# Kernel tuning notes

Measured on AMD Instinct MI355X. Metric: run time of the kernel, lower is better.

Reference implementation:

```python
import jax, jax.numpy as jnp
import numpy as np

# ---- static config (mirrors init_kwargs) ----
B, T, H, W = 1, 3, 64, 64
NHEADS, CH = 4, 64
DIM = NHEADS * CH            # 256 = embed_dim*nheads*dim_mult
PS, WS = 7, 9                # patch size, search window
WSH = WS // 2
K_S, K_A = 16, 8             # search top-k, aggregation top-k
S0 = 2                       # stride0: query grid stride
SCALE = CH ** -0.5
NH, NW = (H - 1) // S0 + 1, (W - 1) // S0 + 1
Q = T * NH * NW              # ntotal queries


def reflect_idx(i, n):
    # dnls reflect_bounds: i<0 -> -i, i>=n -> 2(n-1)-i
    i = jnp.where(i < 0, -i, i)
    return jnp.where(i >= n, 2 * (n - 1) - i, i)


def sepconv(x, dw, pw, b):
    # ConvQKV branch: depthwise 3x3 + pointwise 1x1 (+bias). x: [N,C,H,W]
    y = jax.lax.conv_general_dilated(x, dw, (1, 1), 'SAME',
            dimension_numbers=('NCHW', 'OIHW', 'NCHW'),
            feature_group_count=x.shape[1])
    y = jax.lax.conv_general_dilated(y, pw, (1, 1), 'SAME',
            dimension_numbers=('NCHW', 'OIHW', 'NCHW'))
    return y + b[None, :, None, None]


def setup_inputs() -> dict:
    key = jax.random.key(0)
    ks = jax.random.split(key, 12)
    p = lambda k, s, sc=0.02: jax.random.normal(k, s, jnp.float32) * sc
    z = lambda s: jnp.zeros(s, jnp.float32)
    return {
        'vid':  jax.random.normal(ks[0], (B, T, DIM, H, W), jnp.float32),
        'q_dw': p(ks[1], (DIM, 1, 3, 3), 0.1), 'q_pw': p(ks[2], (DIM, DIM, 1, 1)), 'q_b': z((DIM,)),
        'k_dw': p(ks[3], (DIM, 1, 3, 3), 0.1), 'k_pw': p(ks[4], (DIM, DIM, 1, 1)), 'k_b': z((DIM,)),
        'v_dw': p(ks[5], (DIM, 1, 3, 3), 0.1), 'v_pw': p(ks[6], (DIM, DIM, 1, 1)), 'v_b': z((DIM,)),
        'proj_w': p(ks[7], (DIM, DIM)), 'proj_b': z((DIM,)),
    }


def reference(vid, q_dw, q_pw, q_b, k_dw, k_pw, k_b, v_dw, v_pw, v_b, proj_w, proj_b):
    x = vid.reshape(B * T, DIM, H, W)
    q = (sepconv(x, q_dw, q_pw, q_b) * SCALE).reshape(B, T, NHEADS, CH, H, W)
    k = sepconv(x, k_dw, k_pw, k_b).reshape(B, T, NHEADS, CH, H, W)
    v = sepconv(x, v_dw, v_pw, v_b).reshape(B, T, NHEADS, CH, H, W)

    # ---- non-local patch search (prod_with_heads), spatial window ws x ws, wt=0 ----
    yi, xi = jnp.arange(H), jnp.arange(W)
    ye = reflect_idx(jnp.arange(H + PS - 1), H)   # reflect-extended patch footprint
    xe = reflect_idx(jnp.arange(W + PS - 1), W)

    def offset_dists(dyo, dxo):
        # pixelwise q.k for k shifted by (dyo,dxo) with reflect bounds
        ks_ = k[..., reflect_idx(yi + dyo, H), :][..., reflect_idx(xi + dxo, W)]
        d = jnp.sum(q * ks_, axis=3)              # [B,T,HD,H,W]
        # separable ps x ps patch box-sum (patch anchored top-left)
        de = d[..., ye, :][..., xe]               # [B,T,HD,H+PS-1,W+PS-1]
        dsy = sum(de[..., p:p + H, :] for p in range(PS))
        return sum(dsy[..., p:p + W] for p in range(PS))   # [B,T,HD,H,W]

    offs = jnp.arange(WS) - WSH
    dyg, dxg = jnp.meshgrid(offs, offs, indexing='ij')
    dists_all = jax.vmap(offset_dists)(dyg.ravel(), dxg.ravel())  # [L,B,T,HD,H,W]

    gy, gx = jnp.arange(0, H, S0), jnp.arange(0, W, S0)
    dg = dists_all[..., gy, :][..., gx]           # [L,B,T,HD,NH,NW]
    dists = dg.transpose(1, 3, 2, 4, 5, 0).reshape(B, NHEADS, Q, WS * WS)
    vals, inds = jax.lax.top_k(dists, K_S)        # descending
    attn = jax.nn.softmax(vals, axis=-1)[..., :K_A]  # softmax over k_s, keep top k_a
    inds = inds[..., :K_A]

    # ---- weighted patch sum (wpsum) ----
    tq = jnp.repeat(jnp.arange(T), NH * NW)       # query coords [Q]
    yq = jnp.tile(jnp.repeat(gy, NW), T)
    xq = jnp.tile(jnp.tile(gx, NH), T)
    py = jnp.arange(PS)

    vflat = v.transpose(0, 2, 3, 1, 4, 5).reshape(B, NHEADS, CH, T * H * W)
    dy_k = inds // WS - WSH
    dx_k = inds % WS - WSH

    def gather_bh(vf, li):
        # vf: [CH, T*H*W], li: [Q,PS,PS] -> [CH,Q,PS,PS]
        return vf[:, li]

    acc = jnp.zeros((B, NHEADS, CH, Q, PS, PS), vid.dtype)
    for n in range(K_A):  # small fixed loop over neighbors
        yy = reflect_idx((yq[None, None, :] + dy_k[..., n])[..., None] + py, H)  # [B,HD,Q,PS]
        xx = reflect_idx((xq[None, None, :] + dx_k[..., n])[..., None] + py, W)
        lin = tq[None, None, :, None, None] * (H * W) + yy[..., :, None] * W + xx[..., None, :]
        vp = jax.vmap(jax.vmap(gather_bh))(vflat, lin)        # [B,HD,CH,Q,PS,PS]
        acc = acc + attn[..., n][:, :, None, :, None, None] * vp

    # ---- proj over concatenated heads per (query, patch pixel) ----
    pf = acc.transpose(0, 3, 4, 5, 1, 2).reshape(-1, DIM)     # [(B Q PS PS), DIM]
    pf = pf @ proj_w.T + proj_b

    # ---- iFoldz: overlap-add + per-pixel normalization ----
    patches = pf.reshape(B, Q, PS, PS, DIM).transpose(0, 4, 1, 2, 3)  # [B,DIM,Q,PS,PS]
    yyf = reflect_idx(yq[:, None] + py, H)
    xxf = reflect_idx(xq[:, None] + py, W)
    linf = (tq[:, None, None] * (H * W) + yyf[:, :, None] * W + xxf[:, None, :]).ravel()
    vacc = jnp.zeros((B, DIM, T * H * W), vid.dtype).at[:, :, linf].add(patches.reshape(B, DIM, -1))
    zv = jnp.zeros((T * H * W,), vid.dtype).at[linf].add(1.0)
    out = (vacc / zv).reshape(B, DIM, T, H, W).transpose(0, 2, 1, 3, 4)  # [B,T,DIM,H,W]
    return out
```

## Files before the change

kernel.cpp:

```cpp
#include <hip/hip_runtime.h>
#include <hip/hip_bf16.h>
#include <cmath>

#define TT 3
#define HH 64
#define WW 64
#define NPIX 4096
#define NHEADS 4
#define CHD 64
#define DIMD 256
#define PS 7
#define WS 9
#define WSH 4
#define KS 16
#define KA 8
#define NG 32
#define QTOT 3072
#define NOFF 81
#define SCALE 0.125f

#define OFF_DW   ((size_t)0)
#define OFF_Q    ((size_t)9437184)
#define OFF_K    ((size_t)12582912)
#define OFF_V    ((size_t)15728640)
#define OFF_D    ((size_t)18874368)
#define OFF_DG   ((size_t)22855680)
#define OFF_ATTN ((size_t)23851008)
#define OFF_INDS ((size_t)23949312)
#define OFF_VACC ((size_t)24047616)

__device__ __forceinline__ int reflect_i(int i, int n) {
  i = i < 0 ? -i : i;
  return i >= n ? 2 * (n - 1) - i : i;
}

__global__ void k_dw(const float* __restrict__ vid,
                     const float* __restrict__ qdw, const float* __restrict__ kdw,
                     const float* __restrict__ vdw, float* __restrict__ dw) {
  int plane = blockIdx.x;
  int ch = plane & 255;
  const float* src = vid + (size_t)plane * NPIX;
  float wq[9], wk[9], wv[9];
#pragma unroll
  for (int i = 0; i < 9; i++) { wq[i] = qdw[ch*9+i]; wk[i] = kdw[ch*9+i]; wv[i] = vdw[ch*9+i]; }
  int x = threadIdx.x, ty = threadIdx.y;
  for (int yb = 0; yb < 16; ++yb) {
    int y = yb * 4 + ty;
    float aq = 0, ak = 0, av = 0;
#pragma unroll
    for (int a = 0; a < 3; a++) {
      int yy = y + a - 1;
      if (yy < 0 || yy >= HH) continue;
#pragma unroll
      for (int b = 0; b < 3; b++) {
        int xx = x + b - 1;
        if (xx < 0 || xx >= WW) continue;
        float xv = src[yy * WW + xx];
        aq += xv * wq[a*3+b]; ak += xv * wk[a*3+b]; av += xv * wv[a*3+b];
      }
    }
    size_t o = (size_t)plane * NPIX + y * WW + x;
    dw[o] = aq;
    dw[(size_t)3145728 + o] = ak;
    dw[(size_t)6291456 + o] = av;
  }
}

__global__ void k_pw(const float* __restrict__ dw,
                     const float* __restrict__ qpw, const float* __restrict__ qb,
                     const float* __restrict__ kpw, const float* __restrict__ kb,
                     const float* __restrict__ vpw, const float* __restrict__ vb,
                     float* __restrict__ qo, float* __restrict__ ko, float* __restrict__ vo) {
  int type = blockIdx.z / 3, t = blockIdx.z % 3;
  const float* W   = type == 0 ? qpw : (type == 1 ? kpw : vpw);
  const float* bia = type == 0 ? qb  : (type == 1 ? kb  : vb);
  const float* A = dw + (size_t)type * 3145728 + (size_t)t * 1048576;
  int p0 = blockIdx.x * 64, o0 = blockIdx.y * 64;

  __shared__ float sW[2][16][68];
  __shared__ float sA[2][16][68];

  int tid = threadIdx.x;
  int ty = tid >> 4, tx = tid & 15;
  int wrow = tid >> 2, wcol = tid & 3;
  int arow = tid >> 4, acol = tid & 15;

  const float* Wp = &W[(size_t)(o0 + wrow) * 256 + wcol * 4];
  const float* Ap = &A[(size_t)arow * NPIX + p0 + acol * 4];

  {
    float4 w4 = *(const float4*)Wp;
    float4 a4 = *(const float4*)Ap;
    sW[0][wcol * 4 + 0][wrow] = w4.x;
    sW[0][wcol * 4 + 1][wrow] = w4.y;
    sW[0][wcol * 4 + 2][wrow] = w4.z;
    sW[0][wcol * 4 + 3][wrow] = w4.w;
    *(float4*)&sA[0][arow][acol * 4] = a4;
  }
  float4 wH = *(const float4*)(Wp + 16);
  float4 aH = *(const float4*)(Ap + (size_t)16 * NPIX);
  __syncthreads();

  float acc[4][4] = {};

#pragma unroll 1
  for (int k0 = 0; k0 < 256; k0 += 16) {
    const int cur = (k0 >> 4) & 1;
    float4 wN, aN;
    if (k0 + 32 < 256) {
      wN = *(const float4*)(Wp + k0 + 32);
      aN = *(const float4*)(Ap + (size_t)(k0 + 32) * NPIX);
    }
#pragma unroll
    for (int kk = 0; kk < 16; kk++) {
      float4 av = *(const float4*)&sW[cur][kk][ty * 4];
      float4 bv = *(const float4*)&sA[cur][kk][tx * 4];
      acc[0][0] += av.x * bv.x; acc[0][1] += av.x * bv.y; acc[0][2] += av.x * bv.z; acc[0][3] += av.x * bv.w;
      acc[1][0] += av.y * bv.x; acc[1][1] += av.y * bv.y; acc[1][2] += av.y * bv.z; acc[1][3] += av.y * bv.w;
      acc[2][0] += av.z * bv.x; acc[2][1] += av.z * bv.y; acc[2][2] += av.z * bv.z; acc[2][3] += av.z * bv.w;
      acc[3][0] += av.w * bv.x; acc[3][1] += av.w * bv.y; acc[3][2] += av.w * bv.z; acc[3][3] += av.w * bv.w;
    }
    if (k0 + 16 < 256) {
      const int nxt = cur ^ 1;
      sW[nxt][wcol * 4 + 0][wrow] = wH.x;
      sW[nxt][wcol * 4 + 1][wrow] = wH.y;
      sW[nxt][wcol * 4 + 2][wrow] = wH.z;
      sW[nxt][wcol * 4 + 3][wrow] = wH.w;
      *(float4*)&sA[nxt][arow][acol * 4] = aH;
      __syncthreads();
      wH = wN; aH = aN;
    }
  }

  int obase = o0 + ty * 4, pbase = p0 + tx * 4;
  if (type == 2) {
#pragma unroll
    for (int j = 0; j < 4; j++) {
      float4 ov = make_float4(acc[0][j] + bia[obase + 0],
                              acc[1][j] + bia[obase + 1],
                              acc[2][j] + bia[obase + 2],
                              acc[3][j] + bia[obase + 3]);
      *(float4*)&vo[((size_t)t * NPIX + pbase + j) * 256 + obase] = ov;
    }
  } else {
    float* dst = (type == 0) ? qo : ko;
    float sc = (type == 0) ? SCALE : 1.0f;
#pragma unroll
    for (int i = 0; i < 4; i++) {
      float bb = bia[obase + i];
      float4 ov = make_float4((acc[i][0] + bb) * sc, (acc[i][1] + bb) * sc,
                              (acc[i][2] + bb) * sc, (acc[i][3] + bb) * sc);
      *(float4*)&dst[((size_t)t * 256 + obase + i) * NPIX + pbase] = ov;
    }
  }
}

__global__ void k_dist(const float* __restrict__ q, const float* __restrict__ k,
                       float* __restrict__ D) {
  int b = blockIdx.x;
  int y = b & 63, th = b >> 6;
  int t = th >> 2, h = th & 3;
  __shared__ float4 sK4[16][64];
  int tid = threadIdx.x;
  int x = tid & 63, w = tid >> 6;
  const float* qp = q + ((size_t)t * 256 + h * 64) * NPIX + y * WW;
  const float* kp = k + ((size_t)t * 256 + h * 64) * NPIX;

  float4 qv[16];
#pragma unroll
  for (int cc = 0; cc < 16; cc++) {
    qv[cc].x = qp[(size_t)(4 * cc + 0) * NPIX + x];
    qv[cc].y = qp[(size_t)(4 * cc + 1) * NPIX + x];
    qv[cc].z = qp[(size_t)(4 * cc + 2) * NPIX + x];
    qv[cc].w = qp[(size_t)(4 * cc + 3) * NPIX + x];
  }

  for (int dyi = 0; dyi < 9; ++dyi) {
    int yk = reflect_i(y + dyi - 4, HH);
    __syncthreads();
    {
      int cc = tid >> 6;
      const float* kr = kp + (size_t)yk * WW;
#pragma unroll
      for (int r = 0; r < 4; r++) {
        int c4 = (cc + 4 * r) * 4;
        float4 kv;
        kv.x = kr[(size_t)(c4 + 0) * NPIX + x];
        kv.y = kr[(size_t)(c4 + 1) * NPIX + x];
        kv.z = kr[(size_t)(c4 + 2) * NPIX + x];
        kv.w = kr[(size_t)(c4 + 3) * NPIX + x];
        sK4[cc + 4 * r][x] = kv;
      }
    }
    __syncthreads();
    for (int dxi = w; dxi < 9; dxi += 4) {
      int xk = reflect_i(x + dxi - 4, WW);
      float s0 = 0.f, s1 = 0.f, s2 = 0.f, s3 = 0.f;
#pragma unroll
      for (int cc = 0; cc < 16; cc++) {
        float4 kv = sK4[cc][xk];
        s0 += qv[cc].x * kv.x;
        s1 += qv[cc].y * kv.y;
        s2 += qv[cc].z * kv.z;
        s3 += qv[cc].w * kv.w;
      }
      D[((size_t)(dyi * 9 + dxi) * 12 + th) * NPIX + y * WW + x] = (s0 + s1) + (s2 + s3);
    }
  }
}

__global__ void k_box(const float* __restrict__ D, float* __restrict__ DG) {
  int th = blockIdx.x, n = blockIdx.y;
  int t = th >> 2, h = th & 3;
  __shared__ float sD[4096];
  __shared__ float sR[64][33];
  int tid = threadIdx.x;
  const float* Dp = D + ((size_t)n * 12 + th) * NPIX;
  for (int i = tid; i < 4096; i += 256) sD[i] = Dp[i];
  __syncthreads();
  for (int e = tid; e < 2048; e += 256) {
    int y = e >> 5, gx = e & 31;
    int xq = gx * 2;
    const float* row = sD + y * WW;
    float s = 0.f;
#pragma unroll
    for (int px = 0; px < 7; px++) {
      int rx = xq + px; rx = rx >= WW ? 126 - rx : rx;
      s += row[rx];
    }
    sR[y][gx] = s;
  }
  __syncthreads();
  for (int qi = tid; qi < 1024; qi += 256) {
    int gy = qi >> 5, gx = qi & 31;
    int yq = gy * 2;
    float s = 0.f;
#pragma unroll
    for (int py = 0; py < 7; py++) {
      int ry = yq + py; ry = ry >= HH ? 126 - ry : ry;
      s += sR[ry][gx];
    }
    DG[((size_t)h * QTOT + t * 1024 + qi) * NOFF + n] = s;
  }
}

__global__ void k_topk(const float* __restrict__ DG, float* __restrict__ attn,
                       int* __restrict__ inds) {
  int lane = threadIdx.x & 63;
  int r = blockIdx.x * 4 + (threadIdx.x >> 6);
  const float* row = DG + (size_t)r * NOFF;

  float v0 = row[lane];
  float v1 = (lane < NOFF - 64) ? row[64 + lane] : 0.f;

  auto mono = [](float f) -> unsigned {
    unsigned b = __float_as_uint(f);
    return (b & 0x80000000u) ? ~b : (b | 0x80000000u);
  };
  unsigned long long k0 = ((unsigned long long)mono(v0) << 7) | (unsigned)(127 - lane);
  unsigned long long k1 = (lane < NOFF - 64)
      ? (((unsigned long long)mono(v1) << 7) | (unsigned)(127 - 64 - lane))
      : 0ull;

  float vals[KS]; int idx[KS];
#pragma unroll
  for (int s = 0; s < KS; s++) {
    unsigned long long k = k0 > k1 ? k0 : k1;
#pragma unroll
    for (int m = 32; m >= 1; m >>= 1) {
      unsigned long long o = __shfl_xor(k, m, 64);
      if (o > k) k = o;
    }
    int wi = 127 - (int)(k & 127);
    unsigned mb = (unsigned)(k >> 7);
    unsigned vb = (mb & 0x80000000u) ? (mb ^ 0x80000000u) : ~mb;
    vals[s] = __uint_as_float(vb);
    idx[s] = wi;
    if (wi == lane) k0 = 0ull;
    else if (wi == 64 + lane) k1 = 0ull;
  }

  if (lane == 0) {
    float m = vals[0], den = 0.f, e[KS];
#pragma unroll
    for (int s = 0; s < KS; s++) { e[s] = expf(vals[s] - m); den += e[s]; }
    float inv = 1.f / den;
#pragma unroll
    for (int s = 0; s < KA; s++) {
      attn[(size_t)r * KA + s] = e[s] * inv;
      inds[(size_t)r * KA + s] = idx[s];
    }
  }
}

#define NW 7
__global__ void k_agg(const float* __restrict__ v, const float* __restrict__ attn,
                      const int* __restrict__ inds, float* __restrict__ vacc) {
  int bid = blockIdx.x;
  int swz = (bid & 7) * 384 + (bid >> 3);
  int xg = swz & 15, y = (swz >> 4) & 63, t = swz >> 10;
  int x0 = xg * 4;

  int g0 = max(0, (y - 5) >> 1), g1 = y >> 1;
  int ndir = g1 - g0 + 1;
  int yr = 126 - y;
  int r0 = (yr - 5) >> 1;
  int ny = ndir + (y >= 58 ? (min(31, yr >> 1) - r0 + 1) : 0);

  int gxw0 = max(0, (x0 - 5) >> 1);
  int gxw1 = (x0 + 3) >= 58 ? 31 : ((x0 + 3) >> 1);
  int nw = gxw1 - gxw0 + 1;

  __shared__ float wt[7][NW][4][8];
  __shared__ int2  rc[7][NW][4][8];

  int tid = threadIdx.x;
  {
    int iy = tid / (NW * 4);
    int rem = tid - iy * (NW * 4);
    int gxi = rem >> 2, h = rem & 3;
    if (iy < ny && gxi < nw) {
      int gy, py;
      if (iy < ndir) { gy = g0 + iy; py = y - 2 * gy; }
      else           { gy = r0 + (iy - ndir); py = yr - 2 * gy; }
      int gx = gxw0 + gxi;
      size_t r = (size_t)(h * QTOT + t * 1024 + gy * 32 + gx);
      float4 w0 = *(const float4*)(attn + r * KA);
      float4 w1 = *(const float4*)(attn + r * KA + 4);
      int4 i0 = *(const int4*)(inds + r * KA);
      int4 i1 = *(const int4*)(inds + r * KA + 4);
      int ids[8] = {i0.x, i0.y, i0.z, i0.w, i1.x, i1.y, i1.z, i1.w};
      float ww[8] = {w0.x, w0.y, w0.z, w0.w, w1.x, w1.y, w1.z, w1.w};
#pragma unroll
      for (int n = 0; n < 8; n++) {
        int dy = ids[n] / 9 - 4, dx = ids[n] % 9 - 4;
        int row = 2 * gy + dy + py;
        row = row < 0 ? -row : row;
        row = min(row, 126 - row);
        wt[iy][gxi][h][n] = ww[n];
        rc[iy][gxi][h][n] = make_int2(row << 16, 2 * gx + dx);
      }
    }
  }
  __syncthreads();

  int wv = tid >> 6, lane = tid & 63;
  int x = x0 + wv;
  int h = lane >> 4;
  const char* vB = (const char*)v + (size_t)t * ((size_t)NPIX * DIMD * 4)
                   + (unsigned)(lane * 16);

  int a0 = max(0, (x - 5) >> 1), a1 = x >> 1;
  int xr = 126 - x;
  int b0 = (xr - 5) >> 1, b1 = min(31, xr >> 1);
  bool has_refl = (x >= 58);

  float4 acc = make_float4(0.f, 0.f, 0.f, 0.f);
  for (int iy = 0; iy < ny; ++iy) {
    for (int g = a0; g <= a1; ++g) {
      int gxi = g - gxw0, px = x - 2 * g;
      const float* w8 = wt[iy][gxi][h];
      const int2* r8 = rc[iy][gxi][h];
#pragma unroll
      for (int n = 0; n < 8; n++) {
        float w = w8[n]; int2 e = r8[n];
        int col = e.y + px;
        col = col < 0 ? -col : col;
        col = min(col, 126 - col);
        float4 vv = *(const float4*)(vB + (unsigned)(e.x + (col << 10)));
        acc.x += w * vv.x; acc.y += w * vv.y; acc.z += w * vv.z; acc.w += w * vv.w;
      }
    }
    if (has_refl) {
      for (int g = b0; g <= b1; ++g) {
        int gxi = g - gxw0, px = xr - 2 * g;
        const float* w8 = wt[iy][gxi][h];
        const int2* r8 = rc[iy][gxi][h];
#pragma unroll
        for (int n = 0; n < 8; n++) {
          float w = w8[n]; int2 e = r8[n];
          int col = e.y + px;
          col = col < 0 ? -col : col;
          col = min(col, 126 - col);
          float4 vv = *(const float4*)(vB + (unsigned)(e.x + (col << 10)));
          acc.x += w * vv.x; acc.y += w * vv.y; acc.z += w * vv.z; acc.w += w * vv.w;
        }
      }
    }
  }
  float* oP = vacc + ((size_t)t * NPIX + (size_t)y * WW + x) * DIMD + lane * 4;
  *(float4*)oP = acc;
}

__device__ __forceinline__ int cov_count(int i) {
  int d = (i >> 1) - max(0, (i - 5) >> 1) + 1;
  if (i >= 58) { int r = 126 - i; d += min(31, r >> 1) - ((r - 5) >> 1) + 1; }
  return d;
}

__global__ void k_proj(const float* __restrict__ vacc,
                       const float* __restrict__ pw, const float* __restrict__ pb,
                       float* __restrict__ out) {
  int p0 = blockIdx.x * 64;
  int d0 = blockIdx.y * 64;

  __shared__ float sW[2][16][68];
  __shared__ float sV[2][16][68];

  int tid = threadIdx.x;
  int ty = tid >> 4, tx = tid & 15;
  int row = tid >> 2, col = tid & 3;

  const float* Wp = &pw[(size_t)(d0 + row) * 256 + col * 4];
  const float* Vp = &vacc[(size_t)(p0 + row) * 256 + col * 4];

  {
    float4 w4 = *(const float4*)Wp;
    float4 v4 = *(const float4*)Vp;
    sW[0][col * 4 + 0][row] = w4.x;
    sW[0][col * 4 + 1][row] = w4.y;
    sW[0][col * 4 + 2][row] = w4.z;
    sW[0][col * 4 + 3][row] = w4.w;
    sV[0][col * 4 + 0][row] = v4.x;
    sV[0][col * 4 + 1][row] = v4.y;
    sV[0][col * 4 + 2][row] = v4.z;
    sV[0][col * 4 + 3][row] = v4.w;
  }
  __syncthreads();

  float acc[4][4] = {};

#pragma unroll 1
  for (int k0 = 0; k0 < 256; k0 += 16) {
    const int cur = (k0 >> 4) & 1;
    const bool hn = (k0 + 16) < 256;
    float4 w4n, v4n;
    if (hn) {
      w4n = *(const float4*)(Wp + k0 + 16);
      v4n = *(const float4*)(Vp + k0 + 16);
    }
#pragma unroll
    for (int kk = 0; kk < 16; kk++) {
      float4 av = *(const float4*)&sW[cur][kk][ty * 4];
      float4 bv = *(const float4*)&sV[cur][kk][tx * 4];
      acc[0][0] += av.x * bv.x; acc[0][1] += av.x * bv.y; acc[0][2] += av.x * bv.z; acc[0][3] += av.x * bv.w;
      acc[1][0] += av.y * bv.x; acc[1][1] += av.y * bv.y; acc[1][2] += av.y * bv.z; acc[1][3] += av.y * bv.w;
      acc[2][0] += av.z * bv.x; acc[2][1] += av.z * bv.y; acc[2][2] += av.z * bv.z; acc[2][3] += av.z * bv.w;
      acc[3][0] += av.w * bv.x; acc[3][1] += av.w * bv.y; acc[3][2] += av.w * bv.z; acc[3][3] += av.w * bv.w;
    }
    if (hn) {
      const int nxt = cur ^ 1;
      sW[nxt][col * 4 + 0][row] = w4n.x;
      sW[nxt][col * 4 + 1][row] = w4n.y;
      sW[nxt][col * 4 + 2][row] = w4n.z;
      sW[nxt][col * 4 + 3][row] = w4n.w;
      sV[nxt][col * 4 + 0][row] = v4n.x;
      sV[nxt][col * 4 + 1][row] = v4n.y;
      sV[nxt][col * 4 + 2][row] = v4n.z;
      sV[nxt][col * 4 + 3][row] = v4n.w;
      __syncthreads();
    }
  }

  int dbase = d0 + ty * 4, pbase = p0 + tx * 4;
  float izv[4];
#pragma unroll
  for (int j = 0; j < 4; j++) {
    int pl = (pbase + j) & 4095;
    int yy = pl >> 6, xx = pl & 63;
    izv[j] = 1.0f / (float)(cov_count(yy) * cov_count(xx));
  }
  int t = pbase >> 12, pl0 = pbase & 4095;
#pragma unroll
  for (int i = 0; i < 4; i++) {
    int d = dbase + i;
    float bb = pb[d];
    float4 ov = make_float4(acc[i][0] * izv[0] + bb, acc[i][1] * izv[1] + bb,
                            acc[i][2] * izv[2] + bb, acc[i][3] * izv[3] + bb);
    *(float4*)&out[((size_t)t * 256 + d) * NPIX + pl0] = ov;
  }
}

extern "C" void kernel_launch(void* const* d_in, const int* in_sizes, int n_in,
                              void* d_out, int out_size, void* d_ws, size_t ws_size,
                              hipStream_t stream) {
  const float* vid = (const float*)d_in[0];
  const float* qdw = (const float*)d_in[1];
  const float* qpw = (const float*)d_in[2];
  const float* qb  = (const float*)d_in[3];
  const float* kdw = (const float*)d_in[4];
  const float* kpw = (const float*)d_in[5];
  const float* kb  = (const float*)d_in[6];
  const float* vdw = (const float*)d_in[7];
  const float* vpw = (const float*)d_in[8];
  const float* vb  = (const float*)d_in[9];
  const float* pw  = (const float*)d_in[10];
  const float* pb  = (const float*)d_in[11];
  float* out = (float*)d_out;
  float* ws = (float*)d_ws;

  float* dwb  = ws + OFF_DW;
  float* qbuf = ws + OFF_Q;
  float* kbuf = ws + OFF_K;
  float* vbuf = ws + OFF_V;
  float* Dbuf = ws + OFF_D;
  float* DG   = ws + OFF_DG;
  float* attn = ws + OFF_ATTN;
  int*   inds = (int*)(ws + OFF_INDS);
  float* vacc = ws + OFF_VACC;

  k_dw<<<dim3(768), dim3(64, 4), 0, stream>>>(vid, qdw, kdw, vdw, dwb);
  k_pw<<<dim3(64, 4, 9), 256, 0, stream>>>(dwb, qpw, qb, kpw, kb, vpw, vb,
                                           qbuf, kbuf, vbuf);
  k_dist<<<dim3(768), 256, 0, stream>>>(qbuf, kbuf, Dbuf);
  k_box<<<dim3(12, 81), 256, 0, stream>>>(Dbuf, DG);
  k_topk<<<dim3(3072), 256, 0, stream>>>(DG, attn, inds);
  k_agg<<<dim3(3072), 256, 0, stream>>>(vbuf, attn, inds, vacc);
  k_proj<<<dim3(192, 4), 256, 0, stream>>>(vacc, pw, pb, out);
}
```

Baseline: 244.4 us.

## Deduplicate aggregation gathers by summing attention weights per source pixel in LDS

k_agg now scatter-adds every (query, neighbor) attention weight into a per-(column, head) 16x16 shared-memory weight map keyed by the reflected source pixel. It then builds a compact list of the nonzero cells. The gather loop reads each distinct source pixel once with its summed weight, instead of loading v once per (query, top-k) contribution. The aim is to cut redundant global loads of v, at the cost of LDS zeroing, shared atomics, an extra barrier and a compaction pass. The gather loop runs to the longest list across heads, which adds some lane imbalance.

```diff
diff --git a/kernel.cpp b/kernel.cpp
--- a/kernel.cpp
+++ b/kernel.cpp
@@ -293,7 +293,6 @@
   }
 }
 
-#define NW 7
 __global__ void k_agg(const float* __restrict__ v, const float* __restrict__ attn,
                       const int* __restrict__ inds, float* __restrict__ vacc) {
   int bid = blockIdx.x;
@@ -301,45 +300,67 @@
   int xg = swz & 15, y = (swz >> 4) & 63, t = swz >> 10;
   int x0 = xg * 4;
 
+  int yb = max(0, y - 8);
+  int yr = 126 - y;
+
   int g0 = max(0, (y - 5) >> 1), g1 = y >> 1;
   int ndir = g1 - g0 + 1;
-  int yr = 126 - y;
-  int r0 = (yr - 5) >> 1;
-  int ny = ndir + (y >= 58 ? (min(31, yr >> 1) - r0 + 1) : 0);
-
-  int gxw0 = max(0, (x0 - 5) >> 1);
-  int gxw1 = (x0 + 3) >= 58 ? 31 : ((x0 + 3) >> 1);
-  int nw = gxw1 - gxw0 + 1;
-
-  __shared__ float wt[7][NW][4][8];
-  __shared__ int2  rc[7][NW][4][8];
+  int r0y = (yr - 5) >> 1;
+  int ny = ndir + (y >= 58 ? (min(31, yr >> 1) - r0y + 1) : 0);
+
+  __shared__ float wmap[4][4][257];
+  __shared__ int   lst[4][4][260];
+  __shared__ int   cnt[4][4];
 
   int tid = threadIdx.x;
-  {
-    int iy = tid / (NW * 4);
-    int rem = tid - iy * (NW * 4);
-    int gxi = rem >> 2, h = rem & 3;
-    if (iy < ny && gxi < nw) {
-      int gy, py;
-      if (iy < ndir) { gy = g0 + iy; py = y - 2 * gy; }
-      else           { gy = r0 + (iy - ndir); py = yr - 2 * gy; }
-      int gx = gxw0 + gxi;
-      size_t r = (size_t)(h * QTOT + t * 1024 + gy * 32 + gx);
-      float4 w0 = *(const float4*)(attn + r * KA);
-      float4 w1 = *(const float4*)(attn + r * KA + 4);
-      int4 i0 = *(const int4*)(inds + r * KA);
-      int4 i1 = *(const int4*)(inds + r * KA + 4);
-      int ids[8] = {i0.x, i0.y, i0.z, i0.w, i1.x, i1.y, i1.z, i1.w};
-      float ww[8] = {w0.x, w0.y, w0.z, w0.w, w1.x, w1.y, w1.z, w1.w};
-#pragma unroll
-      for (int n = 0; n < 8; n++) {
-        int dy = ids[n] / 9 - 4, dx = ids[n] % 9 - 4;
-        int row = 2 * gy + dy + py;
-        row = row < 0 ? -row : row;
-        row = min(row, 126 - row);
-        wt[iy][gxi][h][n] = ww[n];
-        rc[iy][gxi][h][n] = make_int2(row << 16, 2 * gx + dx);
-      }
+  for (int i = tid; i < 4 * 4 * 257; i += 256) ((float*)wmap)[i] = 0.f;
+  if (tid < 16) ((int*)cnt)[tid] = 0;
+  __syncthreads();
+
+  int total = 16 * ny * 8;
+  for (int e = tid; e < total; e += 256) {
+    int gs = e & 7;
+    int r = e >> 3;
+    int iy = r % ny; r /= ny;
+    int h = r & 3, xi = r >> 2;
+    int x = x0 + xi;
+    int a0 = max(0, (x - 5) >> 1), a1 = x >> 1;
+    int ndx = a1 - a0 + 1;
+    int xr = 126 - x;
+    int b0x = (xr - 5) >> 1, b1x = min(31, xr >> 1);
+    int nrx = (x >= 58) ? (b1x - b0x + 1) : 0;
+    if (gs >= ndx + nrx) continue;
+    int g, colb;
+    if (gs < ndx) { g = a0 + gs; colb = x; }
+    else          { g = b0x + (gs - ndx); colb = xr; }
+    int gy, rowb;
+    if (iy < ndir) { gy = g0 + iy; rowb = y; }
+    else           { gy = r0y + (iy - ndir); rowb = yr; }
+    size_t rq = (size_t)(h * QTOT + t * 1024 + gy * 32 + g);
+    float4 w0 = *(const float4*)(attn + rq * KA);
+    float4 w1 = *(const float4*)(attn + rq * KA + 4);
+    int4 i0 = *(const int4*)(inds + rq * KA);
+    int4 i1 = *(const int4*)(inds + rq * KA + 4);
+    int ids[8] = {i0.x, i0.y, i0.z, i0.w, i1.x, i1.y, i1.z, i1.w};
+    float ww[8] = {w0.x, w0.y, w0.z, w0.w, w1.x, w1.y, w1.z, w1.w};
+    int xb = max(0, x - 8);
+#pragma unroll
+    for (int n = 0; n < 8; n++) {
+      int dy = ids[n] / 9 - 4, dx = ids[n] % 9 - 4;
+      int rr = reflect_i(rowb + dy, HH);
+      int cc = reflect_i(colb + dx, WW);
+      int cell = ((rr - yb) << 4) | (cc - xb);
+      atomicAdd(&wmap[xi][h][cell], ww[n]);
+    }
+  }
+  __syncthreads();
+
+  for (int e = tid; e < 4096; e += 256) {
+    int cell = e & 255, h = (e >> 8) & 3, xi = e >> 10;
+    float wv_ = wmap[xi][h][cell];
+    if (wv_ != 0.f) {
+      int pos = atomicAdd(&cnt[xi][h], 1);
+      lst[xi][h][pos] = cell;
     }
   }
   __syncthreads();
@@ -347,46 +368,22 @@
   int wv = tid >> 6, lane = tid & 63;
   int x = x0 + wv;
   int h = lane >> 4;
+  int xb = max(0, x - 8);
   const char* vB = (const char*)v + (size_t)t * ((size_t)NPIX * DIMD * 4)
                    + (unsigned)(lane * 16);
-
-  int a0 = max(0, (x - 5) >> 1), a1 = x >> 1;
-  int xr = 126 - x;
-  int b0 = (xr - 5) >> 1, b1 = min(31, xr >> 1);
-  bool has_refl = (x >= 58);
+  int len = cnt[wv][h];
+  int maxlen = max(max(cnt[wv][0], cnt[wv][1]), max(cnt[wv][2], cnt[wv][3]));
+  int rowbase = yb * WW + xb;
 
   float4 acc = make_float4(0.f, 0.f, 0.f, 0.f);
-  for (int iy = 0; iy < ny; ++iy) {
-    for (int g = a0; g <= a1; ++g) {
-      int gxi = g - gxw0, px = x - 2 * g;
-      const float* w8 = wt[iy][gxi][h];
-      const int2* r8 = rc[iy][gxi][h];
-#pragma unroll
-      for (int n = 0; n < 8; n++) {
-        float w = w8[n]; int2 e = r8[n];
-        int col = e.y + px;
-        col = col < 0 ? -col : col;
-        col = min(col, 126 - col);
-        float4 vv = *(const float4*)(vB + (unsigned)(e.x + (col << 10)));
-        acc.x += w * vv.x; acc.y += w * vv.y; acc.z += w * vv.z; acc.w += w * vv.w;
-      }
-    }
-    if (has_refl) {
-      for (int g = b0; g <= b1; ++g) {
-        int gxi = g - gxw0, px = xr - 2 * g;
-        const float* w8 = wt[iy][gxi][h];
-        const int2* r8 = rc[iy][gxi][h];
-#pragma unroll
-        for (int n = 0; n < 8; n++) {
-          float w = w8[n]; int2 e = r8[n];
-          int col = e.y + px;
-          col = col < 0 ? -col : col;
-          col = min(col, 126 - col);
-          float4 vv = *(const float4*)(vB + (unsigned)(e.x + (col << 10)));
-          acc.x += w * vv.x; acc.y += w * vv.y; acc.z += w * vv.z; acc.w += w * vv.w;
-        }
-      }
-    }
+#pragma unroll 4
+  for (int i = 0; i < maxlen; ++i) {
+    int ii = min(i, len - 1);
+    int cell = lst[wv][h][ii];
+    float w = (i < len) ? wmap[wv][h][cell] : 0.f;
+    unsigned off = (unsigned)((rowbase + ((cell >> 4) << 6) + (cell & 15)) << 10);
+    float4 vv = *(const float4*)(vB + off);
+    acc.x += w * vv.x; acc.y += w * vv.y; acc.z += w * vv.z; acc.w += w * vv.w;
   }
   float* oP = vacc + ((size_t)t * NPIX + (size_t)y * WW + x) * DIMD + lane * 4;
   *(float4*)oP = acc;
```

Result: slower. 255.5 us (+4.5%).
